# Kernel optimization log

Hardware: AMD Instinct MI355X
Metric: run time of the kernel (lower is better)

## Reference

```python
import jax, jax.numpy as jnp
import numpy as np

V, E, ENC, D, A = 10000, 512, 2048, 512, 512  # vocab, embed, encoder_dim, decoder_dim, attention_dim
B, L, T = 64, 49, 20


def setup_inputs() -> dict:
    key = jax.random.key(0)
    ks = jax.random.split(key, 20)
    s = lambda k, shape, fan: jax.random.normal(k, shape, jnp.float32) / np.sqrt(fan)
    return {
        "encoder_out": jax.random.normal(ks[0], (B, L, ENC), jnp.float32),
        "captions": jax.random.randint(ks[1], (B, T), 0, V),
        "emb_table": s(ks[2], (V, E), E),
        "W_enc_att": s(ks[3], (ENC, A), ENC), "b_enc_att": jnp.zeros((A,), jnp.float32),
        "W_dec_att": s(ks[4], (D, A), D), "b_dec_att": jnp.zeros((A,), jnp.float32),
        "w_full": s(ks[5], (A,), A), "b_full": jnp.zeros((), jnp.float32),
        "W_ih": s(ks[6], (4 * D, E + ENC), E + ENC), "b_ih": jnp.zeros((4 * D,), jnp.float32),
        "W_hh": s(ks[7], (4 * D, D), D), "b_hh": jnp.zeros((4 * D,), jnp.float32),
        "W_init_h": s(ks[8], (ENC, D), ENC), "b_init_h": jnp.zeros((D,), jnp.float32),
        "W_init_c": s(ks[9], (ENC, D), ENC), "b_init_c": jnp.zeros((D,), jnp.float32),
        "W_out": s(ks[10], (D, V), D), "b_out": jnp.zeros((V,), jnp.float32),
    }


def _decoder(encoder_out, captions, emb_table, W_enc_att, b_enc_att, W_dec_att,
             b_dec_att, w_full, b_full, W_ih, b_ih, W_hh, b_hh,
             W_init_h, b_init_h, W_init_c, b_init_c, W_out, b_out):
    # init hidden/cell from mean encoder features
    mean_enc = encoder_out.mean(axis=1)                      # (B, ENC)
    h = mean_enc @ W_init_h + b_init_h                        # (B, D)
    c = mean_enc @ W_init_c + b_init_c
    # precompute encoder projection for additive attention (shared across steps)
    enc_proj = jnp.einsum('ble,ea->bla', encoder_out, W_enc_att) + b_enc_att  # (B, L, A)
    embeddings = emb_table[captions]                          # (B, T, E)
    emb_seq = jnp.swapaxes(embeddings, 0, 1)                  # (T, B, E)
    Dh = h.shape[-1]

    def step(carry, emb_t):
        h, c = carry
        # additive attention over L=49 locations
        dec_proj = h @ W_dec_att + b_dec_att                  # (B, A)
        att = jax.nn.relu(enc_proj + dec_proj[:, None, :])    # (B, L, A)
        scores = jnp.einsum('bla,a->bl', att, w_full) + b_full
        alpha = jax.nn.softmax(scores, axis=-1)               # (B, L)
        context = jnp.einsum('bl,ble->be', alpha, encoder_out)  # (B, ENC)
        # LSTMCell (PyTorch gate order: i, f, g, o)
        x = jnp.concatenate([emb_t, context], axis=1)         # (B, E+ENC)
        gates = x @ W_ih.T + b_ih + h @ W_hh.T + b_hh         # (B, 4D)
        i, f, g, o = jnp.split(gates, 4, axis=1)
        i, f, o = jax.nn.sigmoid(i), jax.nn.sigmoid(f), jax.nn.sigmoid(o)
        g = jnp.tanh(g)
        c_new = f * c + i * g
        h_new = o * jnp.tanh(c_new)
        # dropout is identity in eval mode
        logits_t = h_new @ W_out + b_out                      # (B, V)
        return (h_new, c_new), (logits_t, alpha)

    (_, _), (logits, alphas) = jax.lax.scan(step, (h, c), emb_seq)
    logits = jnp.swapaxes(logits, 0, 1)                       # (B, T, V)
    alphas = jnp.swapaxes(alphas, 0, 1)                       # (B, T, L)
    return logits, alphas


def reference(encoder_out, captions, emb_table, W_enc_att, b_enc_att, W_dec_att,
              b_dec_att, w_full, b_full, W_ih, b_ih, W_hh, b_hh,
              W_init_h, b_init_h, W_init_c, b_init_c, W_out, b_out):
    return _decoder(encoder_out, captions, emb_table, W_enc_att, b_enc_att,
                    W_dec_att, b_dec_att, w_full, b_full, W_ih, b_ih, W_hh, b_hh,
                    W_init_h, b_init_h, W_init_c, b_init_c, W_out, b_out)
```

## Files before the change

kernel.cpp:

```cpp
#include <hip/hip_runtime.h>
#include <hip/hip_bf16.h>

constexpr int NV   = 10000;
constexpr int NE   = 512;
constexpr int NENC = 2048;
constexpr int ND   = 512;
constexpr int NA   = 512;
constexpr int NB   = 64;
constexpr int NL   = 49;
constexpr int NT   = 20;
constexpr int KX   = NE + NENC + ND;
constexpr int KIH  = NE + NENC;

typedef short bfrag __attribute__((ext_vector_type(8)));
typedef float f32x4 __attribute__((ext_vector_type(4)));

__device__ __forceinline__ float us2f(unsigned short u) {
    union { unsigned int i; float f; } x; x.i = (unsigned int)u << 16; return x.f;
}
__device__ __forceinline__ unsigned short f2us(float f) {
    union { float f_; unsigned int u; } x; x.f_ = f;
    unsigned int r = (x.u + 0x7fffu + ((x.u >> 16) & 1u)) >> 16;
    return (unsigned short)r;
}

__launch_bounds__(256)
__global__ void k_mean(const float* __restrict__ enc, unsigned short* __restrict__ meanbf)
{
    const int b = blockIdx.x;
    const int e = blockIdx.y * 256 + threadIdx.x;
    const float* p = enc + (size_t)b * NL * NENC + e;
    float s = 0.f;
    #pragma unroll 7
    for (int l = 0; l < NL; ++l) s += p[(size_t)l * NENC];
    meanbf[(size_t)b * NENC + e] = f2us(s * (1.0f / NL));
}

__launch_bounds__(256)
__global__ void k_init_mfma(const unsigned short* __restrict__ meanbf,
                            const unsigned short* __restrict__ WicT,
                            const float* __restrict__ bh, const float* __restrict__ bc,
                            unsigned short* __restrict__ hbf, float* __restrict__ c)
{
    const int wave = threadIdx.x >> 6, lane = threadIdx.x & 63;
    const int m0 = wave * 16, n0 = blockIdx.x * 16;
    const int r = lane & 15, quad = lane >> 4;
    const unsigned short* ap = meanbf + (size_t)(m0 + r) * NENC + quad * 8;
    const unsigned short* bp = WicT   + (size_t)(n0 + r) * NENC + quad * 8;
    f32x4 acc = {0.f, 0.f, 0.f, 0.f};
    #pragma unroll 8
    for (int k = 0; k < NENC; k += 32) {
        bfrag a = *(const bfrag*)(ap + k);
        bfrag b = *(const bfrag*)(bp + k);
        acc = __builtin_amdgcn_mfma_f32_16x16x32_bf16(a, b, acc, 0, 0, 0);
    }
    const int n = n0 + r;
    const bool isC = n >= ND;
    const float bv = isC ? bc[n - ND] : bh[n];
    #pragma unroll
    for (int i = 0; i < 4; ++i) {
        int m = m0 + quad * 4 + i;
        float v = acc[i] + bv;
        if (isC) c[(size_t)m * ND + (n - ND)] = v;
        else     hbf[(size_t)m * ND + n] = f2us(v);
    }
}

__launch_bounds__(256)
__global__ void k_cvt3(const float* __restrict__ s0, unsigned short* __restrict__ d0,
                       const float* __restrict__ s1, unsigned short* __restrict__ d1,
                       const float* __restrict__ s2, unsigned short* __restrict__ d2)
{
    int bid = blockIdx.x;
    const float* src; unsigned short* dst;
    if (bid < 6272)       { src = s0; dst = d0; }
    else if (bid < 11392) { src = s1; dst = d1; bid -= 6272; }
    else                  { src = s2; dst = d2; bid -= 11392; }
    const int i = bid * 1024 + threadIdx.x * 4;
    float4 v = *(const float4*)(src + i);
    dst[i + 0] = f2us(v.x); dst[i + 1] = f2us(v.y);
    dst[i + 2] = f2us(v.z); dst[i + 3] = f2us(v.w);
}

__launch_bounds__(256)
__global__ void k_transpose_all(const float* __restrict__ Wh0, const float* __restrict__ Wc0,
                                const float* __restrict__ Wea, const float* __restrict__ Wda,
                                const float* __restrict__ Wout,
                                unsigned short* __restrict__ WicT,
                                unsigned short* __restrict__ WeaT,
                                unsigned short* __restrict__ WdaT,
                                unsigned short* __restrict__ WoutT)
{
    __shared__ float t[32][33];
    int bid = blockIdx.x;
    const float* src; unsigned short* dst; int K, N, nCols;
    if (bid < 1024)      { src = Wh0;  dst = WicT;                       K = NENC; N = ND; nCols = 16; }
    else if (bid < 2048) { src = Wc0;  dst = WicT + (size_t)ND * NENC;   K = NENC; N = ND; nCols = 16; bid -= 1024; }
    else if (bid < 3072) { src = Wea;  dst = WeaT;                       K = NENC; N = NA; nCols = 16; bid -= 2048; }
    else if (bid < 3328) { src = Wda;  dst = WdaT;                       K = ND;   N = NA; nCols = 16; bid -= 3072; }
    else                 { src = Wout; dst = WoutT;                      K = ND;   N = NV; nCols = 313; bid -= 3328; }
    const int nb = (bid % nCols) * 32, kb = (bid / nCols) * 32;
    const int tx = threadIdx.x & 31, ty = threadIdx.x >> 5;
    #pragma unroll
    for (int i = ty; i < 32; i += 8) {
        int n = nb + tx;
        t[i][tx] = (n < N) ? src[(size_t)(kb + i) * N + n] : 0.f;
    }
    __syncthreads();
    #pragma unroll
    for (int i = ty; i < 32; i += 8) {
        int n = nb + i;
        if (n < N) dst[(size_t)n * K + kb + tx] = f2us(t[tx][i]);
    }
}

__launch_bounds__(256)
__global__ void k_encproj_mfma(const unsigned short* __restrict__ encb,
                               const unsigned short* __restrict__ WeaT,
                               const float* __restrict__ bias,
                               unsigned short* __restrict__ epb)
{
    const int j = (blockIdx.x & 7) * 98 + (blockIdx.x >> 3);
    const int ngr = j & 15;
    const int mg  = j >> 4;
    const int wave = threadIdx.x >> 6, lane = threadIdx.x & 63;
    const int wm = wave & 1, wn = wave >> 1;
    const int m0 = mg * 64 + wm * 32;
    const int n0 = ngr * 32 + wn * 16;
    const int r = lane & 15, quad = lane >> 4;
    const unsigned short* ap0 = encb + (size_t)(m0 + r) * NENC + quad * 8;
    const unsigned short* ap1 = ap0 + (size_t)16 * NENC;
    const unsigned short* bp0 = WeaT + (size_t)(n0 + r) * NENC + quad * 8;
    f32x4 acc0 = {0.f,0.f,0.f,0.f}, acc1 = {0.f,0.f,0.f,0.f};
    #pragma unroll 8
    for (int k = 0; k < NENC; k += 32) {
        bfrag a0 = *(const bfrag*)(ap0 + k);
        bfrag a1 = *(const bfrag*)(ap1 + k);
        bfrag b0 = *(const bfrag*)(bp0 + k);
        acc0 = __builtin_amdgcn_mfma_f32_16x16x32_bf16(a0, b0, acc0, 0, 0, 0);
        acc1 = __builtin_amdgcn_mfma_f32_16x16x32_bf16(a1, b0, acc1, 0, 0, 0);
    }
    const float bv = bias[n0 + r];
    #pragma unroll
    for (int i = 0; i < 4; ++i) {
        int ma = m0 + quad * 4 + i;
        epb[(size_t)ma * NA + n0 + r]        = f2us(acc0[i] + bv);
        epb[(size_t)(ma + 16) * NA + n0 + r] = f2us(acc1[i] + bv);
    }
}

__device__ __forceinline__ void logits_tasks(int t, int lo, int hi,
    int worker, int nworkers, int wave, int lane,
    const unsigned short* hbf, const unsigned short* WoutT,
    const float* bout, float* out)
{
    const int slot = wave >> 2, w4 = wave & 3;
    const int r = lane & 15, quad = lane >> 4;
    const int m0 = w4 * 16;
    for (int task = lo + worker * 2 + slot; task < hi; task += nworkers * 2) {
        const int n0 = task * 16;
        const unsigned short* ap = hbf + (size_t)(m0 + r) * ND + quad * 8;
        const unsigned short* bp = WoutT + (size_t)(n0 + r) * ND + quad * 8;
        f32x4 acc = {0.f, 0.f, 0.f, 0.f};
        #pragma unroll
        for (int k = 0; k < ND; k += 32) {
            bfrag a = *(const bfrag*)(ap + k);
            bfrag b = *(const bfrag*)(bp + k);
            acc = __builtin_amdgcn_mfma_f32_16x16x32_bf16(a, b, acc, 0, 0, 0);
        }
        const float bv = bout[n0 + r];
        #pragma unroll
        for (int i = 0; i < 4; ++i) {
            int m = m0 + quad * 4 + i;
            out[((size_t)m * NT + t) * NV + n0 + r] = acc[i] + bv;
        }
    }
}

__device__ __forceinline__ void att_body(int t, int b, int tid,
    const unsigned short* hcur, const unsigned short* epb,
    const unsigned short* encb, const unsigned short* WdaT,
    const float* bda, const float* wf, const float* bfs,
    const float* embt, const int* caps, unsigned short* x, float* alpha_out,
    float* dp , float* al )
{
    const int wave = tid >> 6, lane = tid & 63;
    const int r = lane & 15, quad = lane >> 4;

    x[(size_t)b * KX + NE + NENC + tid] = hcur[(size_t)b * ND + tid];
    const int tok = caps[b * NT + t];
    x[(size_t)b * KX + tid] = f2us(embt[(size_t)tok * NE + tid]);

    {
        const unsigned short* hb_row = hcur + (size_t)b * ND;
        #pragma unroll
        for (int jj = 0; jj < 4; ++jj) {
            const int n0 = (wave * 4 + jj) * 16;
            const unsigned short* bp = WdaT + (size_t)(n0 + r) * ND + quad * 8;
            f32x4 acc = {0.f, 0.f, 0.f, 0.f};
            #pragma unroll
            for (int k = 0; k < ND; k += 32) {
                bfrag a = *(const bfrag*)(hb_row + k + quad * 8);
                bfrag bb = *(const bfrag*)(bp + k);
                acc = __builtin_amdgcn_mfma_f32_16x16x32_bf16(a, bb, acc, 0, 0, 0);
            }
            if (quad == 0) dp[n0 + r] = acc[0] + bda[n0 + r];
        }
    }
    __syncthreads();

    const float bfull = bfs[0];
    for (int l = wave; l < NL; l += 8) {
        const unsigned short* ep = epb + ((size_t)b * NL + l) * NA;
        float s = 0.f;
        #pragma unroll
        for (int a = lane; a < NA; a += 64) {
            float v = us2f(ep[a]) + dp[a];
            v = v > 0.f ? v : 0.f;
            s = fmaf(v, wf[a], s);
        }
        #pragma unroll
        for (int off = 32; off > 0; off >>= 1) s += __shfl_down(s, off, 64);
        if (lane == 0) al[l] = s + bfull;
    }
    __syncthreads();

    if (tid < 64) {
        float v = (tid < NL) ? al[tid] : -1e30f;
        float m = v;
        #pragma unroll
        for (int off = 32; off > 0; off >>= 1) m = fmaxf(m, __shfl_xor(m, off, 64));
        float e = (tid < NL) ? expf(v - m) : 0.f;
        float s = e;
        #pragma unroll
        for (int off = 32; off > 0; off >>= 1) s += __shfl_xor(s, off, 64);
        float a = e / s;
        if (tid < NL) {
            al[tid] = a;
            alpha_out[((size_t)b * NT + t) * NL + tid] = a;
        }
    }
    __syncthreads();

    {
        const int e = tid * 4;
        const unsigned short* p = encb + (size_t)b * NL * NENC + e;
        float s0 = 0.f, s1 = 0.f, s2 = 0.f, s3 = 0.f;
        #pragma unroll 7
        for (int l = 0; l < NL; ++l) {
            ushort4 v = *(const ushort4*)(p + (size_t)l * NENC);
            float a = al[l];
            s0 = fmaf(a, us2f(v.x), s0);
            s1 = fmaf(a, us2f(v.y), s1);
            s2 = fmaf(a, us2f(v.z), s2);
            s3 = fmaf(a, us2f(v.w), s3);
        }
        unsigned short* xo = x + (size_t)b * KX + NE + e;
        xo[0] = f2us(s0); xo[1] = f2us(s1); xo[2] = f2us(s2); xo[3] = f2us(s3);
    }
}

__launch_bounds__(512)
__global__ void k_att_logits(int t,
                             const unsigned short* __restrict__ hcur,
                             const unsigned short* __restrict__ epb,
                             const unsigned short* __restrict__ encb,
                             const unsigned short* __restrict__ WdaT,
                             const float* __restrict__ bda,
                             const float* __restrict__ wf,
                             const float* __restrict__ bfs,
                             const float* __restrict__ embt,
                             const int* __restrict__ captions,
                             unsigned short* __restrict__ x,
                             float* __restrict__ alpha_out,
                             const unsigned short* __restrict__ WoutT,
                             const float* __restrict__ bout,
                             float* __restrict__ out)
{
    __shared__ float smem[576];
    const int bid = blockIdx.x, tid = threadIdx.x;
    if (bid < 64) {
        att_body(t, bid, tid, hcur, epb, encb, WdaT, bda, wf, bfs,
                 embt, captions, x, alpha_out, smem, smem + 512);
    } else if (t > 0) {
        logits_tasks(t - 1, 0, 384, bid - 64, 192, tid >> 6, tid & 63,
                     hcur, WoutT, bout, out);
    }
}

__launch_bounds__(512)
__global__ void k_gates_lstm(int t,
                             const unsigned short* __restrict__ x,
                             const unsigned short* __restrict__ Wihb,
                             const unsigned short* __restrict__ Whhb,
                             const float* __restrict__ bih, const float* __restrict__ bhh,
                             unsigned short* __restrict__ hnxt, float* __restrict__ c,
                             const unsigned short* __restrict__ hcur,
                             const unsigned short* __restrict__ WoutT,
                             const float* __restrict__ bout,
                             float* __restrict__ out)
{
    __shared__ float part[8 * 4 * 16 * 16];
    const int bid = blockIdx.x;
    const int wave = threadIdx.x >> 6, lane = threadIdx.x & 63;
    if (bid >= 128) {
        if (t > 0)
            logits_tasks(t - 1, 384, 625, bid - 128, 121, wave, lane,
                         hcur, WoutT, bout, out);
        return;
    }
    const int ng = (bid & 7) * 4 + ((bid >> 3) & 3);
    const int mt = bid >> 5;
    const int m0 = mt * 16, n0 = ng * 16;
    const int r = lane & 15, quad = lane >> 4;
    const int k0 = wave * (KX / 8), k1 = k0 + (KX / 8);

    const unsigned short* ap = x + (size_t)(m0 + r) * KX + quad * 8;
    const unsigned short* bpih[4];
    const unsigned short* bphh[4];
    #pragma unroll
    for (int g = 0; g < 4; ++g) {
        bpih[g] = Wihb + (size_t)(g * ND + n0 + r) * KIH + quad * 8;
        bphh[g] = Whhb + (size_t)(g * ND + n0 + r) * ND + quad * 8;
    }
    f32x4 acc[4] = {{0.f,0.f,0.f,0.f},{0.f,0.f,0.f,0.f},
                    {0.f,0.f,0.f,0.f},{0.f,0.f,0.f,0.f}};

    const int kiA = (k1 < KIH) ? k1 : KIH;
    #pragma unroll 4
    for (int k = k0; k < kiA; k += 32) {
        bfrag a = *(const bfrag*)(ap + k);
        #pragma unroll
        for (int g = 0; g < 4; ++g) {
            bfrag b = *(const bfrag*)(bpih[g] + k);
            acc[g] = __builtin_amdgcn_mfma_f32_16x16x32_bf16(a, b, acc[g], 0, 0, 0);
        }
    }
    const int kiB = (k0 > KIH) ? k0 : KIH;
    #pragma unroll 4
    for (int k = kiB; k < k1; k += 32) {
        bfrag a = *(const bfrag*)(ap + k);
        #pragma unroll
        for (int g = 0; g < 4; ++g) {
            bfrag b = *(const bfrag*)(bphh[g] + (k - KIH));
            acc[g] = __builtin_amdgcn_mfma_f32_16x16x32_bf16(a, b, acc[g], 0, 0, 0);
        }
    }

    #pragma unroll
    for (int g = 0; g < 4; ++g)
        #pragma unroll
        for (int i = 0; i < 4; ++i)
            part[((wave * 4 + g) * 16 + quad * 4 + i) * 16 + r] = acc[g][i];
    __syncthreads();

    if (threadIdx.x < 256) {
        const int row = threadIdx.x >> 4, col = threadIdx.x & 15;
        float gs[4];
        #pragma unroll
        for (int g = 0; g < 4; ++g) {
            float v = 0.f;
            #pragma unroll
            for (int w = 0; w < 8; ++w)
                v += part[((w * 4 + g) * 16 + row) * 16 + col];
            gs[g] = v;
        }
        const int d = n0 + col;
        const int m = m0 + row;
        float gi = gs[0] + bih[d]        + bhh[d];
        float gf = gs[1] + bih[d + 512]  + bhh[d + 512];
        float gg = gs[2] + bih[d + 1024] + bhh[d + 1024];
        float go = gs[3] + bih[d + 1536] + bhh[d + 1536];
        float ig = 1.f / (1.f + expf(-gi));
        float fg = 1.f / (1.f + expf(-gf));
        float g  = tanhf(gg);
        float og = 1.f / (1.f + expf(-go));
        float cn = fg * c[(size_t)m * ND + d] + ig * g;
        float hn = og * tanhf(cn);
        c[(size_t)m * ND + d] = cn;
        hnxt[(size_t)m * ND + d] = f2us(hn);
    }
}

__launch_bounds__(512)
__global__ void k_logits_fin(int t,
                             const unsigned short* __restrict__ hbf,
                             const unsigned short* __restrict__ WoutT,
                             const float* __restrict__ bout,
                             float* __restrict__ out)
{
    logits_tasks(t, 0, 625, blockIdx.x, 313, threadIdx.x >> 6, threadIdx.x & 63,
                 hbf, WoutT, bout, out);
}

extern "C" void kernel_launch(void* const* d_in, const int* in_sizes, int n_in,
                              void* d_out, int out_size, void* d_ws, size_t ws_size,
                              hipStream_t stream) {
    const float* enc  = (const float*)d_in[0];
    const int*   caps = (const int*)d_in[1];
    const float* embt = (const float*)d_in[2];
    const float* Wea  = (const float*)d_in[3];
    const float* bea  = (const float*)d_in[4];
    const float* Wda  = (const float*)d_in[5];
    const float* bda  = (const float*)d_in[6];
    const float* wf   = (const float*)d_in[7];
    const float* bfs  = (const float*)d_in[8];
    const float* Wih  = (const float*)d_in[9];
    const float* bih  = (const float*)d_in[10];
    const float* Whh  = (const float*)d_in[11];
    const float* bhh  = (const float*)d_in[12];
    const float* Wh0  = (const float*)d_in[13];
    const float* bh0  = (const float*)d_in[14];
    const float* Wc0  = (const float*)d_in[15];
    const float* bc0  = (const float*)d_in[16];
    const float* Wout = (const float*)d_in[17];
    const float* bout = (const float*)d_in[18];

    float* out = (float*)d_out;
    float* alpha_out = out + (size_t)NB * NT * NV;

    char* w = (char*)d_ws;
    float* c     = (float*)w;                 w += (size_t)NB * ND * 4;
    unsigned short* meanbf = (unsigned short*)w; w += (size_t)NB * NENC * 2;
    unsigned short* hb    = (unsigned short*)w; w += (size_t)2 * NB * ND * 2;
    unsigned short* x     = (unsigned short*)w; w += (size_t)NB * KX * 2;
    unsigned short* epb   = (unsigned short*)w; w += (size_t)NB * NL * NA * 2;
    unsigned short* encb  = (unsigned short*)w; w += (size_t)NB * NL * NENC * 2;
    unsigned short* Wihb  = (unsigned short*)w; w += (size_t)4 * ND * KIH * 2;
    unsigned short* Whhb  = (unsigned short*)w; w += (size_t)4 * ND * ND * 2;
    unsigned short* WeaT  = (unsigned short*)w; w += (size_t)NA * NENC * 2;
    unsigned short* WdaT  = (unsigned short*)w; w += (size_t)NA * ND * 2;
    unsigned short* WoutT = (unsigned short*)w; w += (size_t)NV * ND * 2;
    unsigned short* WicT  = (unsigned short*)w; w += (size_t)2 * ND * NENC * 2;

    hipLaunchKernelGGL(k_mean, dim3(NB, NENC / 256), dim3(256), 0, stream, enc, meanbf);
    hipLaunchKernelGGL(k_cvt3, dim3(12416), dim3(256), 0, stream,
                       enc, encb, Wih, Wihb, Whh, Whhb);
    hipLaunchKernelGGL(k_transpose_all, dim3(8336), dim3(256), 0, stream,
                       Wh0, Wc0, Wea, Wda, Wout, WicT, WeaT, WdaT, WoutT);
    hipLaunchKernelGGL(k_init_mfma, dim3(2 * ND / 16), dim3(256), 0, stream,
                       meanbf, WicT, bh0, bc0, hb, c);
    hipLaunchKernelGGL(k_encproj_mfma, dim3(784), dim3(256), 0, stream,
                       encb, WeaT, bea, epb);

    for (int t = 0; t < NT; ++t) {
        unsigned short* hcur = hb + (size_t)(t & 1) * NB * ND;
        unsigned short* hnxt = hb + (size_t)((t + 1) & 1) * NB * ND;
        hipLaunchKernelGGL(k_att_logits, dim3(256), dim3(512), 0, stream,
                           t, hcur, epb, encb, WdaT, bda, wf, bfs, embt, caps,
                           x, alpha_out, WoutT, bout, out);
        hipLaunchKernelGGL(k_gates_lstm, dim3(249), dim3(512), 0, stream,
                           t, x, Wihb, Whhb, bih, bhh, hnxt, c,
                           hcur, WoutT, bout, out);
    }
    hipLaunchKernelGGL(k_logits_fin, dim3(313), dim3(512), 0, stream,
                       NT - 1, hb + (size_t)(NT & 1) * NB * ND, WoutT, bout, out);
}
```

Baseline: 1.153 ms.

## Merge prep kernels, split-K encoder projection, hoist decoder attention projection

Merges the mean, conversion and transpose kernels into a single prep launch. Combines the encoder-projection and init-state GEMMs into one launch that uses 512 threads, larger tiles and split-K with a shared-memory reduction. Moves the per-batch decoder attention projection out of the attention blocks into a separate small batched MFMA kernel launched after each LSTM step. The goal is to cut redundant per-block weight reads in attention and reduce launch count, at the cost of one extra launch per timestep.

```diff
diff --git a/kernel.cpp b/kernel.cpp
--- a/kernel.cpp
+++ b/kernel.cpp
@@ -25,127 +25,156 @@
 }
 
 __launch_bounds__(256)
-__global__ void k_mean(const float* __restrict__ enc, unsigned short* __restrict__ meanbf)
-{
-    const int b = blockIdx.x;
-    const int e = blockIdx.y * 256 + threadIdx.x;
-    const float* p = enc + (size_t)b * NL * NENC + e;
-    float s = 0.f;
-    #pragma unroll 7
-    for (int l = 0; l < NL; ++l) s += p[(size_t)l * NENC];
-    meanbf[(size_t)b * NENC + e] = f2us(s * (1.0f / NL));
-}
-
-__launch_bounds__(256)
-__global__ void k_init_mfma(const unsigned short* __restrict__ meanbf,
-                            const unsigned short* __restrict__ WicT,
-                            const float* __restrict__ bh, const float* __restrict__ bc,
-                            unsigned short* __restrict__ hbf, float* __restrict__ c)
-{
-    const int wave = threadIdx.x >> 6, lane = threadIdx.x & 63;
-    const int m0 = wave * 16, n0 = blockIdx.x * 16;
+__global__ void k_prep(const float* __restrict__ enc, unsigned short* __restrict__ encb,
+                       const float* __restrict__ Wih, unsigned short* __restrict__ Wihb,
+                       const float* __restrict__ Whh, unsigned short* __restrict__ Whhb,
+                       const float* __restrict__ Wh0, const float* __restrict__ Wc0,
+                       const float* __restrict__ Wea, const float* __restrict__ Wda,
+                       const float* __restrict__ Wout,
+                       unsigned short* __restrict__ WicT, unsigned short* __restrict__ WeaT,
+                       unsigned short* __restrict__ WdaT, unsigned short* __restrict__ WoutT,
+                       unsigned short* __restrict__ meanbf)
+{
+    int bid = blockIdx.x;
+    if (bid < 12416) {
+        const float* src; unsigned short* dst;
+        if (bid < 6272)       { src = enc; dst = encb; }
+        else if (bid < 11392) { src = Wih; dst = Wihb; bid -= 6272; }
+        else                  { src = Whh; dst = Whhb; bid -= 11392; }
+        const int i = bid * 1024 + threadIdx.x * 4;
+        float4 v = *(const float4*)(src + i);
+        dst[i + 0] = f2us(v.x); dst[i + 1] = f2us(v.y);
+        dst[i + 2] = f2us(v.z); dst[i + 3] = f2us(v.w);
+    } else if (bid < 20752) {
+        bid -= 12416;
+        __shared__ float t[32][33];
+        const float* src; unsigned short* dst; int K, N, nCols;
+        if (bid < 1024)      { src = Wh0;  dst = WicT;                     K = NENC; N = ND; nCols = 16; }
+        else if (bid < 2048) { src = Wc0;  dst = WicT + (size_t)ND * NENC; K = NENC; N = ND; nCols = 16; bid -= 1024; }
+        else if (bid < 3072) { src = Wea;  dst = WeaT;                     K = NENC; N = NA; nCols = 16; bid -= 2048; }
+        else if (bid < 3328) { src = Wda;  dst = WdaT;                     K = ND;   N = NA; nCols = 16; bid -= 3072; }
+        else                 { src = Wout; dst = WoutT;                    K = ND;   N = NV; nCols = 313; bid -= 3328; }
+        const int nb = (bid % nCols) * 32, kb = (bid / nCols) * 32;
+        const int tx = threadIdx.x & 31, ty = threadIdx.x >> 5;
+        #pragma unroll
+        for (int i = ty; i < 32; i += 8) {
+            int n = nb + tx;
+            t[i][tx] = (n < N) ? src[(size_t)(kb + i) * N + n] : 0.f;
+        }
+        __syncthreads();
+        #pragma unroll
+        for (int i = ty; i < 32; i += 8) {
+            int n = nb + i;
+            if (n < N) dst[(size_t)n * K + kb + tx] = f2us(t[tx][i]);
+        }
+    } else {
+        bid -= 20752;
+        const int b = bid >> 3;
+        const int e = (bid & 7) * 256 + threadIdx.x;
+        const float* p = enc + (size_t)b * NL * NENC + e;
+        float s = 0.f;
+        #pragma unroll 7
+        for (int l = 0; l < NL; ++l) s += p[(size_t)l * NENC];
+        meanbf[(size_t)b * NENC + e] = f2us(s * (1.0f / NL));
+    }
+}
+
+__launch_bounds__(512)
+__global__ void k_mfma2(const unsigned short* __restrict__ encb,
+                        const unsigned short* __restrict__ WeaT,
+                        const float* __restrict__ bea,
+                        unsigned short* __restrict__ epb,
+                        const unsigned short* __restrict__ meanbf,
+                        const unsigned short* __restrict__ WicT,
+                        const float* __restrict__ bh, const float* __restrict__ bc,
+                        unsigned short* __restrict__ hbf, float* __restrict__ c)
+{
+    __shared__ float comb[4 * 64 * 16];
+    const int tid = threadIdx.x;
+    const int wave = tid >> 6, lane = tid & 63;
     const int r = lane & 15, quad = lane >> 4;
-    const unsigned short* ap = meanbf + (size_t)(m0 + r) * NENC + quad * 8;
-    const unsigned short* bp = WicT   + (size_t)(n0 + r) * NENC + quad * 8;
-    f32x4 acc = {0.f, 0.f, 0.f, 0.f};
-    #pragma unroll 8
-    for (int k = 0; k < NENC; k += 32) {
-        bfrag a = *(const bfrag*)(ap + k);
-        bfrag b = *(const bfrag*)(bp + k);
-        acc = __builtin_amdgcn_mfma_f32_16x16x32_bf16(a, b, acc, 0, 0, 0);
-    }
-    const int n = n0 + r;
-    const bool isC = n >= ND;
-    const float bv = isC ? bc[n - ND] : bh[n];
-    #pragma unroll
-    for (int i = 0; i < 4; ++i) {
-        int m = m0 + quad * 4 + i;
-        float v = acc[i] + bv;
-        if (isC) c[(size_t)m * ND + (n - ND)] = v;
-        else     hbf[(size_t)m * ND + n] = f2us(v);
-    }
-}
-
-__launch_bounds__(256)
-__global__ void k_cvt3(const float* __restrict__ s0, unsigned short* __restrict__ d0,
-                       const float* __restrict__ s1, unsigned short* __restrict__ d1,
-                       const float* __restrict__ s2, unsigned short* __restrict__ d2)
-{
-    int bid = blockIdx.x;
-    const float* src; unsigned short* dst;
-    if (bid < 6272)       { src = s0; dst = d0; }
-    else if (bid < 11392) { src = s1; dst = d1; bid -= 6272; }
-    else                  { src = s2; dst = d2; bid -= 11392; }
-    const int i = bid * 1024 + threadIdx.x * 4;
-    float4 v = *(const float4*)(src + i);
-    dst[i + 0] = f2us(v.x); dst[i + 1] = f2us(v.y);
-    dst[i + 2] = f2us(v.z); dst[i + 3] = f2us(v.w);
-}
-
-__launch_bounds__(256)
-__global__ void k_transpose_all(const float* __restrict__ Wh0, const float* __restrict__ Wc0,
-                                const float* __restrict__ Wea, const float* __restrict__ Wda,
-                                const float* __restrict__ Wout,
-                                unsigned short* __restrict__ WicT,
-                                unsigned short* __restrict__ WeaT,
-                                unsigned short* __restrict__ WdaT,
-                                unsigned short* __restrict__ WoutT)
-{
-    __shared__ float t[32][33];
-    int bid = blockIdx.x;
-    const float* src; unsigned short* dst; int K, N, nCols;
-    if (bid < 1024)      { src = Wh0;  dst = WicT;                       K = NENC; N = ND; nCols = 16; }
-    else if (bid < 2048) { src = Wc0;  dst = WicT + (size_t)ND * NENC;   K = NENC; N = ND; nCols = 16; bid -= 1024; }
-    else if (bid < 3072) { src = Wea;  dst = WeaT;                       K = NENC; N = NA; nCols = 16; bid -= 2048; }
-    else if (bid < 3328) { src = Wda;  dst = WdaT;                       K = ND;   N = NA; nCols = 16; bid -= 3072; }
-    else                 { src = Wout; dst = WoutT;                      K = ND;   N = NV; nCols = 313; bid -= 3328; }
-    const int nb = (bid % nCols) * 32, kb = (bid / nCols) * 32;
-    const int tx = threadIdx.x & 31, ty = threadIdx.x >> 5;
-    #pragma unroll
-    for (int i = ty; i < 32; i += 8) {
-        int n = nb + tx;
-        t[i][tx] = (n < N) ? src[(size_t)(kb + i) * N + n] : 0.f;
-    }
-    __syncthreads();
-    #pragma unroll
-    for (int i = ty; i < 32; i += 8) {
-        int n = nb + i;
-        if (n < N) dst[(size_t)n * K + kb + tx] = f2us(t[tx][i]);
-    }
-}
-
-__launch_bounds__(256)
-__global__ void k_encproj_mfma(const unsigned short* __restrict__ encb,
-                               const unsigned short* __restrict__ WeaT,
-                               const float* __restrict__ bias,
-                               unsigned short* __restrict__ epb)
-{
-    const int j = (blockIdx.x & 7) * 98 + (blockIdx.x >> 3);
-    const int ngr = j & 15;
-    const int mg  = j >> 4;
-    const int wave = threadIdx.x >> 6, lane = threadIdx.x & 63;
-    const int wm = wave & 1, wn = wave >> 1;
-    const int m0 = mg * 64 + wm * 32;
-    const int n0 = ngr * 32 + wn * 16;
-    const int r = lane & 15, quad = lane >> 4;
-    const unsigned short* ap0 = encb + (size_t)(m0 + r) * NENC + quad * 8;
-    const unsigned short* ap1 = ap0 + (size_t)16 * NENC;
-    const unsigned short* bp0 = WeaT + (size_t)(n0 + r) * NENC + quad * 8;
-    f32x4 acc0 = {0.f,0.f,0.f,0.f}, acc1 = {0.f,0.f,0.f,0.f};
-    #pragma unroll 8
-    for (int k = 0; k < NENC; k += 32) {
-        bfrag a0 = *(const bfrag*)(ap0 + k);
-        bfrag a1 = *(const bfrag*)(ap1 + k);
-        bfrag b0 = *(const bfrag*)(bp0 + k);
-        acc0 = __builtin_amdgcn_mfma_f32_16x16x32_bf16(a0, b0, acc0, 0, 0, 0);
-        acc1 = __builtin_amdgcn_mfma_f32_16x16x32_bf16(a1, b0, acc1, 0, 0, 0);
-    }
-    const float bv = bias[n0 + r];
-    #pragma unroll
-    for (int i = 0; i < 4; ++i) {
-        int ma = m0 + quad * 4 + i;
-        epb[(size_t)ma * NA + n0 + r]        = f2us(acc0[i] + bv);
-        epb[(size_t)(ma + 16) * NA + n0 + r] = f2us(acc1[i] + bv);
+    if (blockIdx.x < 392) {
+        const int j = ((int)blockIdx.x & 7) * 49 + ((int)blockIdx.x >> 3);
+        const int ng = j & 7, mg = j >> 3;
+        const int ow = wave & 3, kh = wave >> 2;
+        const int wm = ow >> 1, wn = ow & 1;
+        const int m0 = mg * 64 + wm * 32;
+        const int n0 = ng * 64 + wn * 32;
+        const int kb = kh * (NENC / 2);
+        const unsigned short* ap0 = encb + (size_t)(m0 + r) * NENC + kb + quad * 8;
+        const unsigned short* ap1 = ap0 + (size_t)16 * NENC;
+        const unsigned short* bp0 = WeaT + (size_t)(n0 + r) * NENC + kb + quad * 8;
+        const unsigned short* bp1 = bp0 + (size_t)16 * NENC;
+        f32x4 a00 = {0.f,0.f,0.f,0.f}, a01 = {0.f,0.f,0.f,0.f};
+        f32x4 a10 = {0.f,0.f,0.f,0.f}, a11 = {0.f,0.f,0.f,0.f};
+        #pragma unroll 4
+        for (int k = 0; k < NENC / 2; k += 32) {
+            bfrag x0 = *(const bfrag*)(ap0 + k);
+            bfrag x1 = *(const bfrag*)(ap1 + k);
+            bfrag y0 = *(const bfrag*)(bp0 + k);
+            bfrag y1 = *(const bfrag*)(bp1 + k);
+            a00 = __builtin_amdgcn_mfma_f32_16x16x32_bf16(x0, y0, a00, 0, 0, 0);
+            a01 = __builtin_amdgcn_mfma_f32_16x16x32_bf16(x0, y1, a01, 0, 0, 0);
+            a10 = __builtin_amdgcn_mfma_f32_16x16x32_bf16(x1, y0, a10, 0, 0, 0);
+            a11 = __builtin_amdgcn_mfma_f32_16x16x32_bf16(x1, y1, a11, 0, 0, 0);
+        }
+        if (kh == 1) {
+            float* d = comb + (ow * 64 + lane) * 16;
+            #pragma unroll
+            for (int i = 0; i < 4; ++i) {
+                d[i]      = a00[i];
+                d[4 + i]  = a01[i];
+                d[8 + i]  = a10[i];
+                d[12 + i] = a11[i];
+            }
+        }
+        __syncthreads();
+        if (kh == 0) {
+            const float* d = comb + (ow * 64 + lane) * 16;
+            const float bv0 = bea[n0 + r], bv1 = bea[n0 + 16 + r];
+            #pragma unroll
+            for (int i = 0; i < 4; ++i) {
+                int ma = m0 + quad * 4 + i, mb = ma + 16;
+                epb[(size_t)ma * NA + n0 + r]      = f2us(a00[i] + d[i]      + bv0);
+                epb[(size_t)ma * NA + n0 + 16 + r] = f2us(a01[i] + d[4 + i]  + bv1);
+                epb[(size_t)mb * NA + n0 + r]      = f2us(a10[i] + d[8 + i]  + bv0);
+                epb[(size_t)mb * NA + n0 + 16 + r] = f2us(a11[i] + d[12 + i] + bv1);
+            }
+        }
+    } else {
+        const int nt = (int)blockIdx.x - 392;
+        const int n0 = nt * 16;
+        const int mtile = wave & 3, kh = wave >> 2;
+        const int m0 = mtile * 16;
+        const int kb = kh * (NENC / 2);
+        const unsigned short* ap = meanbf + (size_t)(m0 + r) * NENC + kb + quad * 8;
+        const unsigned short* bp = WicT   + (size_t)(n0 + r) * NENC + kb + quad * 8;
+        f32x4 acc = {0.f, 0.f, 0.f, 0.f};
+        #pragma unroll 4
+        for (int k = 0; k < NENC / 2; k += 32) {
+            bfrag a = *(const bfrag*)(ap + k);
+            bfrag b = *(const bfrag*)(bp + k);
+            acc = __builtin_amdgcn_mfma_f32_16x16x32_bf16(a, b, acc, 0, 0, 0);
+        }
+        if (kh == 1) {
+            float* d = comb + (mtile * 64 + lane) * 4;
+            #pragma unroll
+            for (int i = 0; i < 4; ++i) d[i] = acc[i];
+        }
+        __syncthreads();
+        if (kh == 0) {
+            const float* d = comb + (mtile * 64 + lane) * 4;
+            const int n = n0 + r;
+            const bool isC = n >= ND;
+            const float bv = isC ? bc[n - ND] : bh[n];
+            #pragma unroll
+            for (int i = 0; i < 4; ++i) {
+                int m = m0 + quad * 4 + i;
+                float v = acc[i] + d[i] + bv;
+                if (isC) c[(size_t)m * ND + (n - ND)] = v;
+                else     hbf[(size_t)m * ND + n] = f2us(v);
+            }
+        }
     }
 }
 
@@ -178,37 +207,18 @@
 }
 
 __device__ __forceinline__ void att_body(int t, int b, int tid,
-    const unsigned short* hcur, const unsigned short* epb,
-    const unsigned short* encb, const unsigned short* WdaT,
-    const float* bda, const float* wf, const float* bfs,
+    const unsigned short* hcur, const float* dpg, const unsigned short* epb,
+    const unsigned short* encb, const float* wf, const float* bfs,
     const float* embt, const int* caps, unsigned short* x, float* alpha_out,
     float* dp , float* al )
 {
-    const int wave = tid >> 6, lane = tid & 63;
-    const int r = lane & 15, quad = lane >> 4;
-
     x[(size_t)b * KX + NE + NENC + tid] = hcur[(size_t)b * ND + tid];
+    dp[tid] = dpg[(size_t)b * NA + tid];
     const int tok = caps[b * NT + t];
     x[(size_t)b * KX + tid] = f2us(embt[(size_t)tok * NE + tid]);
-
-    {
-        const unsigned short* hb_row = hcur + (size_t)b * ND;
-        #pragma unroll
-        for (int jj = 0; jj < 4; ++jj) {
-            const int n0 = (wave * 4 + jj) * 16;
-            const unsigned short* bp = WdaT + (size_t)(n0 + r) * ND + quad * 8;
-            f32x4 acc = {0.f, 0.f, 0.f, 0.f};
-            #pragma unroll
-            for (int k = 0; k < ND; k += 32) {
-                bfrag a = *(const bfrag*)(hb_row + k + quad * 8);
-                bfrag bb = *(const bfrag*)(bp + k);
-                acc = __builtin_amdgcn_mfma_f32_16x16x32_bf16(a, bb, acc, 0, 0, 0);
-            }
-            if (quad == 0) dp[n0 + r] = acc[0] + bda[n0 + r];
-        }
-    }
     __syncthreads();
 
+    const int wave = tid >> 6, lane = tid & 63;
     const float bfull = bfs[0];
     for (int l = wave; l < NL; l += 8) {
         const unsigned short* ep = epb + ((size_t)b * NL + l) * NA;
@@ -263,10 +273,9 @@
 __launch_bounds__(512)
 __global__ void k_att_logits(int t,
                              const unsigned short* __restrict__ hcur,
+                             const float* __restrict__ dpg,
                              const unsigned short* __restrict__ epb,
                              const unsigned short* __restrict__ encb,
-                             const unsigned short* __restrict__ WdaT,
-                             const float* __restrict__ bda,
                              const float* __restrict__ wf,
                              const float* __restrict__ bfs,
                              const float* __restrict__ embt,
@@ -280,7 +289,7 @@
     __shared__ float smem[576];
     const int bid = blockIdx.x, tid = threadIdx.x;
     if (bid < 64) {
-        att_body(t, bid, tid, hcur, epb, encb, WdaT, bda, wf, bfs,
+        att_body(t, bid, tid, hcur, dpg, epb, encb, wf, bfs,
                  embt, captions, x, alpha_out, smem, smem + 512);
     } else if (t > 0) {
         logits_tasks(t - 1, 0, 384, bid - 64, 192, tid >> 6, tid & 63,
@@ -379,6 +388,33 @@
         float hn = og * tanhf(cn);
         c[(size_t)m * ND + d] = cn;
         hnxt[(size_t)m * ND + d] = f2us(hn);
+    }
+}
+
+__launch_bounds__(512)
+__global__ void k_decproj(const unsigned short* __restrict__ hbf,
+                          const unsigned short* __restrict__ WdaT,
+                          const float* __restrict__ bda, float* __restrict__ dp)
+{
+    const int wave = threadIdx.x >> 6, lane = threadIdx.x & 63;
+    const int slot = wave >> 2, w4 = wave & 3;
+    const int tile = blockIdx.x * 2 + slot;
+    const int n0 = tile * 16, m0 = w4 * 16;
+    const int r = lane & 15, quad = lane >> 4;
+    const unsigned short* ap = hbf + (size_t)(m0 + r) * ND + quad * 8;
+    const unsigned short* bp = WdaT + (size_t)(n0 + r) * ND + quad * 8;
+    f32x4 acc = {0.f, 0.f, 0.f, 0.f};
+    #pragma unroll
+    for (int k = 0; k < ND; k += 32) {
+        bfrag a = *(const bfrag*)(ap + k);
+        bfrag b = *(const bfrag*)(bp + k);
+        acc = __builtin_amdgcn_mfma_f32_16x16x32_bf16(a, b, acc, 0, 0, 0);
+    }
+    const float bv = bda[n0 + r];
+    #pragma unroll
+    for (int i = 0; i < 4; ++i) {
+        int m = m0 + quad * 4 + i;
+        dp[(size_t)m * NA + n0 + r] = acc[i] + bv;
     }
 }
 
@@ -421,6 +457,7 @@
 
     char* w = (char*)d_ws;
     float* c     = (float*)w;                 w += (size_t)NB * ND * 4;
+    float* dp    = (float*)w;                 w += (size_t)NB * NA * 4;
     unsigned short* meanbf = (unsigned short*)w; w += (size_t)NB * NENC * 2;
     unsigned short* hb    = (unsigned short*)w; w += (size_t)2 * NB * ND * 2;
     unsigned short* x     = (unsigned short*)w; w += (size_t)NB * KX * 2;
@@ -433,25 +470,25 @@
     unsigned short* WoutT = (unsigned short*)w; w += (size_t)NV * ND * 2;
     unsigned short* WicT  = (unsigned short*)w; w += (size_t)2 * ND * NENC * 2;
 
-    hipLaunchKernelGGL(k_mean, dim3(NB, NENC / 256), dim3(256), 0, stream, enc, meanbf);
-    hipLaunchKernelGGL(k_cvt3, dim3(12416), dim3(256), 0, stream,
-                       enc, encb, Wih, Wihb, Whh, Whhb);
-    hipLaunchKernelGGL(k_transpose_all, dim3(8336), dim3(256), 0, stream,
-                       Wh0, Wc0, Wea, Wda, Wout, WicT, WeaT, WdaT, WoutT);
-    hipLaunchKernelGGL(k_init_mfma, dim3(2 * ND / 16), dim3(256), 0, stream,
-                       meanbf, WicT, bh0, bc0, hb, c);
-    hipLaunchKernelGGL(k_encproj_mfma, dim3(784), dim3(256), 0, stream,
-                       encb, WeaT, bea, epb);
+    hipLaunchKernelGGL(k_prep, dim3(21264), dim3(256), 0, stream,
+                       enc, encb, Wih, Wihb, Whh, Whhb,
+                       Wh0, Wc0, Wea, Wda, Wout, WicT, WeaT, WdaT, WoutT, meanbf);
+    hipLaunchKernelGGL(k_mfma2, dim3(456), dim3(512), 0, stream,
+                       encb, WeaT, bea, epb, meanbf, WicT, bh0, bc0, hb, c);
+    hipLaunchKernelGGL(k_decproj, dim3(16), dim3(512), 0, stream, hb, WdaT, bda, dp);
 
     for (int t = 0; t < NT; ++t) {
         unsigned short* hcur = hb + (size_t)(t & 1) * NB * ND;
         unsigned short* hnxt = hb + (size_t)((t + 1) & 1) * NB * ND;
         hipLaunchKernelGGL(k_att_logits, dim3(256), dim3(512), 0, stream,
-                           t, hcur, epb, encb, WdaT, bda, wf, bfs, embt, caps,
+                           t, hcur, dp, epb, encb, wf, bfs, embt, caps,
                            x, alpha_out, WoutT, bout, out);
         hipLaunchKernelGGL(k_gates_lstm, dim3(249), dim3(512), 0, stream,
                            t, x, Wihb, Whhb, bih, bhh, hnxt, c,
                            hcur, WoutT, bout, out);
+        if (t + 1 < NT)
+            hipLaunchKernelGGL(k_decproj, dim3(16), dim3(512), 0, stream,
+                               hnxt, WdaT, bda, dp);
     }
     hipLaunchKernelGGL(k_logits_fin, dim3(313), dim3(512), 0, stream,
                        NT - 1, hb + (size_t)(NT & 1) * NB * ND, WoutT, bout, out);
```

New measurement: 963.5 us. 1.2x faster.
